# Performance work log

Hardware: AMD Instinct MI355X
Metric: run time of the kernel (lower is better)

## Reference

```python
import jax, jax.numpy as jnp
import numpy as np

B, L, D, H = 2, 384, 256, 8
DH = D // H


def setup_inputs() -> dict:
    key = jax.random.key(0)
    ks = jax.random.split(key, 16)
    xav = lambda k, shape: jax.random.normal(k, shape, jnp.float32) * np.sqrt(2.0 / sum(shape[-2:]))
    return {
        "key": jax.random.normal(ks[0], (B, L, D), jnp.float32),
        "query": jax.random.normal(ks[1], (B, L, D), jnp.float32),
        "value": jax.random.normal(ks[2], (B, L, D), jnp.float32),
        "pos": jax.random.normal(ks[3], (B, L, L, D), jnp.float32),
        "key_mask": jnp.ones((B, L), jnp.float32),
        "Wk": xav(ks[4], (D, D)), "bk": jnp.zeros((D,), jnp.float32),
        "Wq": xav(ks[5], (D, D)), "bq": jnp.zeros((D,), jnp.float32),
        "Wv": xav(ks[6], (D, D)), "bv": jnp.zeros((D,), jnp.float32),
        "Wr": xav(ks[7], (D, D)), "br": jnp.zeros((D,), jnp.float32),
        "u": xav(ks[8], (H, DH)),
        "v": xav(ks[9], (H, DH)),
    }


def reference(key, query, value, pos, key_mask, Wk, bk, Wq, bq, Wv, bv, Wr, br, u, v):
    b, l, d = key.shape
    dh = d // H
    # projections (torch Linear: x @ W.T + b)
    k = (key @ Wk.T + bk).reshape(b, l, H, dh).transpose(0, 2, 1, 3)    # [b,h,l,dh]
    q = (query @ Wq.T + bq).reshape(b, l, H, dh).transpose(0, 2, 1, 3)  # [b,h,l,dh]
    val = (value @ Wv.T + bv).reshape(b, l, H, dh).transpose(0, 2, 1, 3)
    r = (pos @ Wr.T + br).reshape(b, l, l, H, dh)                       # [b,q,k,h,dh]
    # content term A+C: (q + u) @ k^T
    A_C = jnp.einsum("bhqd,bhkd->bhqk", q + u[None, :, None, :], k)
    # position term B+D: (q + v) contracted with per-(q,k) relative embedding
    B_D = jnp.einsum("bhqd,bqkhd->bhqk", q + v[None, :, None, :], r)
    score = (A_C + B_D) / np.sqrt(dh).astype(np.float32)
    score = score - (1.0 - key_mask[:, None, None, :]) * 1e15
    attn = jax.nn.softmax(score, axis=-1)  # dropout is identity at eval
    out = jnp.einsum("bhqk,bhkd->bhqd", attn, val)
    return out.transpose(0, 2, 1, 3).reshape(b, l, d)
```

## Files before the change

kernel.cpp:

```cpp
#include <hip/hip_runtime.h>
#include <math.h>

#define BB 2
#define LL 384
#define DD 256
#define HH 8
#define DHH 32

static const size_t OFF_Q     = 0;
static const size_t OFF_KK    = 196608;
static const size_t OFF_VV    = 393216;
static const size_t OFF_W     = 589824;
static const size_t OFF_CBR   = 2162688;
static const size_t OFF_SCORE = 2168832;

__device__ __forceinline__ float dot4(float4 a, float4 b) {
    return a.x * b.x + a.y * b.y + a.z * b.z + a.w * b.w;
}

__global__ __launch_bounds__(256) void k_proj(
    const float* __restrict__ Xq, const float* __restrict__ Xk, const float* __restrict__ Xv,
    const float* __restrict__ Wq, const float* __restrict__ Wk, const float* __restrict__ Wv,
    const float* __restrict__ bq, const float* __restrict__ bk, const float* __restrict__ bv,
    float* __restrict__ oq, float* __restrict__ okk, float* __restrict__ ovv)
{
    int bx = blockIdx.x;
    int mat = bx / 96;
    int rem = bx % 96;
    int b = rem / 48;
    int l0 = (rem % 48) * 8;
    const float* X = (mat == 0) ? Xq : (mat == 1) ? Xk : Xv;
    const float* W = (mat == 0) ? Wq : (mat == 1) ? Wk : Wv;
    const float* bias = (mat == 0) ? bq : (mat == 1) ? bk : bv;

    __shared__ float xs[8 * 256];
    int tid = threadIdx.x;
    {
        const float4* src = (const float4*)(X + (size_t)(b * LL + l0) * DD);
        float4* dst = (float4*)xs;
        dst[tid] = src[tid];
        dst[tid + 256] = src[tid + 256];
    }
    __syncthreads();

    int n = tid;
    float bn = bias[n];
    float acc[8];
#pragma unroll
    for (int l = 0; l < 8; ++l) acc[l] = bn;

    const float4* wrow = (const float4*)(W + (size_t)n * DD);
#pragma unroll 8
    for (int kc = 0; kc < 64; ++kc) {
        float4 wv = wrow[kc];
#pragma unroll
        for (int l = 0; l < 8; ++l) {
            float4 xv = ((const float4*)(xs + l * 256))[kc];
            acc[l] += dot4(wv, xv);
        }
    }

    if (mat == 0) {
#pragma unroll
        for (int l = 0; l < 8; ++l)
            oq[(size_t)(b * LL + l0 + l) * DD + n] = acc[l];
    } else {
        float* o = (mat == 1) ? okk : ovv;
        int h = n >> 5, dh = n & 31;
#pragma unroll
        for (int l = 0; l < 8; ++l)
            o[((size_t)(b * HH + h) * LL + l0 + l) * DHH + dh] = acc[l];
    }
}

__global__ __launch_bounds__(256) void k_wproj(
    const float* __restrict__ q, const float* __restrict__ vpar,
    const float* __restrict__ Wr, const float* __restrict__ br,
    float* __restrict__ w, float* __restrict__ cbr)
{
    int b = blockIdx.x / 96;
    int l0 = (blockIdx.x % 96) * 4;
    int tid = threadIdx.x;
    int gq = tid >> 6;
    int lane = tid & 63;

    __shared__ float qv[4][256];
    {
        const float4* qsrc = (const float4*)(q + (size_t)(b * LL + l0 + gq) * DD);
        const float4* vsrc = (const float4*)vpar;
        float4 t = qsrc[lane];
        float4 vv4 = vsrc[lane];
        t.x += vv4.x; t.y += vv4.y; t.z += vv4.z; t.w += vv4.w;
        ((float4*)qv[gq])[lane] = t;
    }
    __syncthreads();

    int l = l0 + gq;
    int d4 = lane * 4;
    float* wbase = w + ((size_t)(b * LL + l) * HH) * DD + d4;
    for (int h = 0; h < HH; ++h) {
        float4 acc = make_float4(0.f, 0.f, 0.f, 0.f);
#pragma unroll 8
        for (int dh = 0; dh < 32; ++dh) {
            float s = qv[gq][h * 32 + dh];
            float4 wr4 = *(const float4*)(Wr + (size_t)(h * 32 + dh) * DD + d4);
            acc.x += s * wr4.x; acc.y += s * wr4.y; acc.z += s * wr4.z; acc.w += s * wr4.w;
        }
        *(float4*)(wbase + h * DD) = acc;
    }

    if (tid < 32) {
        int g2 = tid >> 3, hh = tid & 7;
        float s = 0.f;
#pragma unroll 8
        for (int dh = 0; dh < 32; ++dh)
            s += qv[g2][hh * 32 + dh] * br[hh * 32 + dh];
        cbr[(size_t)(b * LL + l0 + g2) * HH + hh] = s;
    }
}

__global__ __launch_bounds__(256) void k_bd(
    const float* __restrict__ pos, const float* __restrict__ w,
    float* __restrict__ score)
{
    int b = blockIdx.x / LL;
    int qi = blockIdx.x % LL;
    int tid = threadIdx.x;
    int wave = tid >> 6;
    int lane = tid & 63;
    int g = lane & 15;
    int r = lane >> 4;

    const float* wb = w + ((size_t)(b * LL + qi) * HH) * DD + g * 4;
    float4 wr[8][4];
#pragma unroll
    for (int h = 0; h < 8; ++h) {
#pragma unroll
        for (int j = 0; j < 4; ++j)
            wr[h][j] = *(const float4*)(wb + h * DD + j * 64);
    }

    const float* posq = pos + (size_t)(b * LL + qi) * LL * DD + g * 4;
    float* sb = score + ((size_t)(b * HH) * LL + qi) * LL;
    const float inv = 0.17677669529663687f;

#pragma unroll 1
    for (int k0 = wave * 4; k0 < LL; k0 += 16) {
        int krow = k0 + r;
        const float* pr = posq + (size_t)krow * DD;
        float4 p0 = *(const float4*)(pr);
        float4 p1 = *(const float4*)(pr + 64);
        float4 p2 = *(const float4*)(pr + 128);
        float4 p3 = *(const float4*)(pr + 192);
        float acc[8];
#pragma unroll
        for (int h = 0; h < 8; ++h)
            acc[h] = dot4(p0, wr[h][0]) + dot4(p1, wr[h][1]) +
                     dot4(p2, wr[h][2]) + dot4(p3, wr[h][3]);
#pragma unroll
        for (int m = 1; m <= 8; m <<= 1) {
#pragma unroll
            for (int h = 0; h < 8; ++h)
                acc[h] += __shfl_xor(acc[h], m, 64);
        }
        if (g == 0) {
#pragma unroll
            for (int h = 0; h < 8; ++h)
                sb[(size_t)h * LL * LL + krow] = acc[h] * inv;
        }
    }
}

__global__ __launch_bounds__(384) void k_ac(
    const float* __restrict__ q, const float* __restrict__ u,
    const float* __restrict__ kk, const float* __restrict__ cbr,
    const float* __restrict__ mask, float* __restrict__ score)
{
    int bx = blockIdx.x;
    int qt = bx & 15;
    int bh = bx >> 4;
    int b = bh >> 3;
    int h = bh & 7;
    int q0 = qt * 24;
    int tid = threadIdx.x;

    __shared__ float qu[24][32];
    __shared__ float cb[24];
    for (int idx = tid; idx < 768; idx += 384) {
        int ql = idx >> 5, dh = idx & 31;
        qu[ql][dh] = q[(size_t)(b * LL + q0 + ql) * DD + h * 32 + dh] + u[h * 32 + dh];
    }
    if (tid < 24) cb[tid] = cbr[(size_t)(b * LL + q0 + tid) * HH + h];

    float4 kr[8];
    const float4* kbase = (const float4*)(kk + ((size_t)(b * HH + h) * LL + tid) * DHH);
#pragma unroll
    for (int j = 0; j < 8; ++j) kr[j] = kbase[j];
    float pen = (1.0f - mask[b * LL + tid]) * 1e15f;
    __syncthreads();

    const float inv = 0.17677669529663687f;
    float* srow = score + ((size_t)(b * HH + h) * LL + q0) * LL + tid;
    for (int ql = 0; ql < 24; ++ql) {
        const float4* qp = (const float4*)qu[ql];
        float acc = 0.f;
#pragma unroll
        for (int j = 0; j < 8; ++j) acc += dot4(qp[j], kr[j]);
        float* sp = srow + (size_t)ql * LL;
        *sp = *sp + (acc + cb[ql]) * inv - pen;
    }
}

__global__ __launch_bounds__(256) void k_softpv(
    const float* __restrict__ score, const float* __restrict__ vv,
    float* __restrict__ out)
{
    int bx = blockIdx.x;
    int qt = bx % 48;
    int bh = bx / 48;
    int b = bh >> 3;
    int h = bh & 7;
    int q0 = qt * 8;
    int tid = threadIdx.x;

    __shared__ float valT[32][388];
    __shared__ float attn[8][388];

    const float* vb = vv + (size_t)(b * HH + h) * LL * DHH;
    for (int i = 0; i < 48; ++i) {
        int flat = i * 256 + tid;
        valT[flat & 31][flat >> 5] = vb[flat];
    }

    int wave = tid >> 6, lane = tid & 63;
    for (int ri = 0; ri < 2; ++ri) {
        int ql = wave * 2 + ri;
        const float* srow = score + ((size_t)(b * HH + h) * LL + q0 + ql) * LL;
        float s[6];
#pragma unroll
        for (int j = 0; j < 6; ++j) s[j] = srow[lane + 64 * j];
        float m = s[0];
#pragma unroll
        for (int j = 1; j < 6; ++j) m = fmaxf(m, s[j]);
#pragma unroll
        for (int off = 1; off < 64; off <<= 1) m = fmaxf(m, __shfl_xor(m, off, 64));
        float e[6];
        float ls = 0.f;
#pragma unroll
        for (int j = 0; j < 6; ++j) { e[j] = __expf(s[j] - m); ls += e[j]; }
#pragma unroll
        for (int off = 1; off < 64; off <<= 1) ls += __shfl_xor(ls, off, 64);
        float rinv = 1.0f / ls;
#pragma unroll
        for (int j = 0; j < 6; ++j) attn[ql][lane + 64 * j] = e[j] * rinv;
    }
    __syncthreads();

    int dh = tid & 31, qp = tid >> 5;
    const float4* vrow = (const float4*)valT[dh];
    const float4* arow = (const float4*)attn[qp];
    float acc = 0.f;
    for (int k4 = 0; k4 < 96; ++k4) {
        acc += dot4(arow[k4], vrow[k4]);
    }
    out[(size_t)(b * LL + q0 + qp) * DD + h * 32 + dh] = acc;
}

extern "C" void kernel_launch(void* const* d_in, const int* in_sizes, int n_in,
                              void* d_out, int out_size, void* d_ws, size_t ws_size,
                              hipStream_t stream) {
    const float* key    = (const float*)d_in[0];
    const float* query  = (const float*)d_in[1];
    const float* value  = (const float*)d_in[2];
    const float* pos    = (const float*)d_in[3];
    const float* kmask  = (const float*)d_in[4];
    const float* Wk     = (const float*)d_in[5];
    const float* bk     = (const float*)d_in[6];
    const float* Wq     = (const float*)d_in[7];
    const float* bq     = (const float*)d_in[8];
    const float* Wv     = (const float*)d_in[9];
    const float* bv     = (const float*)d_in[10];
    const float* Wr     = (const float*)d_in[11];
    const float* br     = (const float*)d_in[12];
    const float* u      = (const float*)d_in[13];
    const float* v      = (const float*)d_in[14];
    float* out = (float*)d_out;

    float* ws = (float*)d_ws;
    float* qbuf   = ws + OFF_Q;
    float* kkbuf  = ws + OFF_KK;
    float* vvbuf  = ws + OFF_VV;
    float* wbuf   = ws + OFF_W;
    float* cbrbuf = ws + OFF_CBR;
    float* sbuf   = ws + OFF_SCORE;

    k_proj<<<dim3(288), dim3(256), 0, stream>>>(query, key, value, Wq, Wk, Wv,
                                                bq, bk, bv, qbuf, kkbuf, vvbuf);
    k_wproj<<<dim3(192), dim3(256), 0, stream>>>(qbuf, v, Wr, br, wbuf, cbrbuf);
    k_bd<<<dim3(768), dim3(256), 0, stream>>>(pos, wbuf, sbuf);
    k_ac<<<dim3(256), dim3(384), 0, stream>>>(qbuf, u, kkbuf, cbrbuf, kmask, sbuf);
    k_softpv<<<dim3(768), dim3(256), 0, stream>>>(sbuf, vvbuf, out);
}
```

Before: 496.1 us.

## Fuse position scores, content scores, softmax and PV into one per-query kernel

Merges the B+D position-score kernel, the A+C content-score kernel and the softmax/PV kernel into a single kernel with one block per (batch, query). The full 8x384 score tile stays in shared memory instead of going through a global score buffer, which removes that buffer's writes and read-modify-writes plus two launches. In exchange, each block re-reads K and V for its query straight from global memory (relying on cache) rather than sharing them across query tiles. The PV loop now reads V with strided scalar loads instead of from a transposed shared-memory copy.

```diff
diff --git a/kernel.cpp b/kernel.cpp
--- a/kernel.cpp
+++ b/kernel.cpp
@@ -7,12 +7,11 @@
 #define HH 8
 #define DHH 32
 
-static const size_t OFF_Q     = 0;
-static const size_t OFF_KK    = 196608;
-static const size_t OFF_VV    = 393216;
-static const size_t OFF_W     = 589824;
-static const size_t OFF_CBR   = 2162688;
-static const size_t OFF_SCORE = 2168832;
+static const size_t OFF_Q   = 0;
+static const size_t OFF_KK  = 196608;
+static const size_t OFF_VV  = 393216;
+static const size_t OFF_W   = 589824;
+static const size_t OFF_CBR = 2162688;
 
 __device__ __forceinline__ float dot4(float4 a, float4 b) {
     return a.x * b.x + a.y * b.y + a.z * b.z + a.w * b.w;
@@ -119,9 +118,12 @@
     }
 }
 
-__global__ __launch_bounds__(256) void k_bd(
+__global__ __launch_bounds__(256, 3) void k_fused(
     const float* __restrict__ pos, const float* __restrict__ w,
-    float* __restrict__ score)
+    const float* __restrict__ q, const float* __restrict__ u,
+    const float* __restrict__ kk, const float* __restrict__ vv,
+    const float* __restrict__ cbr, const float* __restrict__ mask,
+    float* __restrict__ out)
 {
     int b = blockIdx.x / LL;
     int qi = blockIdx.x % LL;
@@ -131,6 +133,11 @@
     int g = lane & 15;
     int r = lane >> 4;
 
+    __shared__ float sc[HH][LL];
+    __shared__ float qu[DD];
+
+    const float inv = 0.17677669529663687f;
+
     const float* wb = w + ((size_t)(b * LL + qi) * HH) * DD + g * 4;
     float4 wr[8][4];
 #pragma unroll
@@ -140,10 +147,28 @@
             wr[h][j] = *(const float4*)(wb + h * DD + j * 64);
     }
 
+    qu[tid] = q[(size_t)(b * LL + qi) * DD + tid] + u[tid];
+    __syncthreads();
+
+    {
+        int h = tid >> 5;
+        int kb = (tid & 31) * 12;
+        float cb = cbr[(size_t)(b * LL + qi) * HH + h];
+        const float4* qp = (const float4*)(qu + h * 32);
+#pragma unroll 2
+        for (int j = 0; j < 12; ++j) {
+            int k = kb + j;
+            const float4* krow = (const float4*)(kk + ((size_t)(b * HH + h) * LL + k) * DHH);
+            float acc = 0.f;
+#pragma unroll
+            for (int jj = 0; jj < 8; ++jj) acc += dot4(qp[jj], krow[jj]);
+            float pen = (1.0f - mask[b * LL + k]) * 1e15f;
+            sc[h][k] = (acc + cb) * inv - pen;
+        }
+    }
+    __syncthreads();
+
     const float* posq = pos + (size_t)(b * LL + qi) * LL * DD + g * 4;
-    float* sb = score + ((size_t)(b * HH) * LL + qi) * LL;
-    const float inv = 0.17677669529663687f;
-
 #pragma unroll 1
     for (int k0 = wave * 4; k0 < LL; k0 += 16) {
         int krow = k0 + r;
@@ -166,79 +191,17 @@
         if (g == 0) {
 #pragma unroll
             for (int h = 0; h < 8; ++h)
-                sb[(size_t)h * LL * LL + krow] = acc[h] * inv;
-        }
-    }
-}
-
-__global__ __launch_bounds__(384) void k_ac(
-    const float* __restrict__ q, const float* __restrict__ u,
-    const float* __restrict__ kk, const float* __restrict__ cbr,
-    const float* __restrict__ mask, float* __restrict__ score)
-{
-    int bx = blockIdx.x;
-    int qt = bx & 15;
-    int bh = bx >> 4;
-    int b = bh >> 3;
-    int h = bh & 7;
-    int q0 = qt * 24;
-    int tid = threadIdx.x;
-
-    __shared__ float qu[24][32];
-    __shared__ float cb[24];
-    for (int idx = tid; idx < 768; idx += 384) {
-        int ql = idx >> 5, dh = idx & 31;
-        qu[ql][dh] = q[(size_t)(b * LL + q0 + ql) * DD + h * 32 + dh] + u[h * 32 + dh];
-    }
-    if (tid < 24) cb[tid] = cbr[(size_t)(b * LL + q0 + tid) * HH + h];
-
-    float4 kr[8];
-    const float4* kbase = (const float4*)(kk + ((size_t)(b * HH + h) * LL + tid) * DHH);
-#pragma unroll
-    for (int j = 0; j < 8; ++j) kr[j] = kbase[j];
-    float pen = (1.0f - mask[b * LL + tid]) * 1e15f;
-    __syncthreads();
-
-    const float inv = 0.17677669529663687f;
-    float* srow = score + ((size_t)(b * HH + h) * LL + q0) * LL + tid;
-    for (int ql = 0; ql < 24; ++ql) {
-        const float4* qp = (const float4*)qu[ql];
-        float acc = 0.f;
-#pragma unroll
-        for (int j = 0; j < 8; ++j) acc += dot4(qp[j], kr[j]);
-        float* sp = srow + (size_t)ql * LL;
-        *sp = *sp + (acc + cb[ql]) * inv - pen;
-    }
-}
-
-__global__ __launch_bounds__(256) void k_softpv(
-    const float* __restrict__ score, const float* __restrict__ vv,
-    float* __restrict__ out)
-{
-    int bx = blockIdx.x;
-    int qt = bx % 48;
-    int bh = bx / 48;
-    int b = bh >> 3;
-    int h = bh & 7;
-    int q0 = qt * 8;
-    int tid = threadIdx.x;
-
-    __shared__ float valT[32][388];
-    __shared__ float attn[8][388];
-
-    const float* vb = vv + (size_t)(b * HH + h) * LL * DHH;
-    for (int i = 0; i < 48; ++i) {
-        int flat = i * 256 + tid;
-        valT[flat & 31][flat >> 5] = vb[flat];
-    }
-
-    int wave = tid >> 6, lane = tid & 63;
+                sc[h][krow] += acc[h] * inv;
+        }
+    }
+    __syncthreads();
+
+#pragma unroll
     for (int ri = 0; ri < 2; ++ri) {
-        int ql = wave * 2 + ri;
-        const float* srow = score + ((size_t)(b * HH + h) * LL + q0 + ql) * LL;
+        int h = wave * 2 + ri;
         float s[6];
 #pragma unroll
-        for (int j = 0; j < 6; ++j) s[j] = srow[lane + 64 * j];
+        for (int j = 0; j < 6; ++j) s[j] = sc[h][lane + 64 * j];
         float m = s[0];
 #pragma unroll
         for (int j = 1; j < 6; ++j) m = fmaxf(m, s[j]);
@@ -252,18 +215,25 @@
         for (int off = 1; off < 64; off <<= 1) ls += __shfl_xor(ls, off, 64);
         float rinv = 1.0f / ls;
 #pragma unroll
-        for (int j = 0; j < 6; ++j) attn[ql][lane + 64 * j] = e[j] * rinv;
-    }
-    __syncthreads();
-
-    int dh = tid & 31, qp = tid >> 5;
-    const float4* vrow = (const float4*)valT[dh];
-    const float4* arow = (const float4*)attn[qp];
-    float acc = 0.f;
-    for (int k4 = 0; k4 < 96; ++k4) {
-        acc += dot4(arow[k4], vrow[k4]);
-    }
-    out[(size_t)(b * LL + q0 + qp) * DD + h * 32 + dh] = acc;
+        for (int j = 0; j < 6; ++j) sc[h][lane + 64 * j] = e[j] * rinv;
+    }
+    __syncthreads();
+
+    {
+        int h = tid >> 5, dh = tid & 31;
+        const float* vb = vv + ((size_t)(b * HH + h) * LL) * DHH + dh;
+        float acc = 0.f;
+#pragma unroll 1
+        for (int k = 0; k < LL; k += 4) {
+            float v0 = vb[(size_t)(k + 0) * DHH];
+            float v1 = vb[(size_t)(k + 1) * DHH];
+            float v2 = vb[(size_t)(k + 2) * DHH];
+            float v3 = vb[(size_t)(k + 3) * DHH];
+            acc += sc[h][k + 0] * v0 + sc[h][k + 1] * v1 +
+                   sc[h][k + 2] * v2 + sc[h][k + 3] * v3;
+        }
+        out[(size_t)(b * LL + qi) * DD + h * 32 + dh] = acc;
+    }
 }
 
 extern "C" void kernel_launch(void* const* d_in, const int* in_sizes, int n_in,
@@ -292,12 +262,10 @@
     float* vvbuf  = ws + OFF_VV;
     float* wbuf   = ws + OFF_W;
     float* cbrbuf = ws + OFF_CBR;
-    float* sbuf   = ws + OFF_SCORE;
 
     k_proj<<<dim3(288), dim3(256), 0, stream>>>(query, key, value, Wq, Wk, Wv,
                                                 bq, bk, bv, qbuf, kkbuf, vvbuf);
     k_wproj<<<dim3(192), dim3(256), 0, stream>>>(qbuf, v, Wr, br, wbuf, cbrbuf);
-    k_bd<<<dim3(768), dim3(256), 0, stream>>>(pos, wbuf, sbuf);
-    k_ac<<<dim3(256), dim3(384), 0, stream>>>(qbuf, u, kkbuf, cbrbuf, kmask, sbuf);
-    k_softpv<<<dim3(768), dim3(256), 0, stream>>>(sbuf, vvbuf, out);
-}
+    k_fused<<<dim3(768), dim3(256), 0, stream>>>(pos, wbuf, qbuf, u, kkbuf, vvbuf,
+                                                 cbrbuf, kmask, out);
+}
```

New measurement: 555.9 us. +12.1%, slower.
